# Kernel tuning notes

Measured on AMD Instinct MI355X. Metric: run time of the kernel, lower is better.

Reference implementation:

```python
import jax, jax.numpy as jnp
import numpy as np

N = 200000          # nodes
E = 800000          # edges (avg degree ~4, molecular graphs)
F_IN = 128          # dataset.num_node_features
HID = 32            # hidden_channels -> widths 32, 64, 128
N_TASKS = 128       # dataset.num_tasks
G = 8000            # number of graphs in the batch
EPS = 1e-5


def _glorot(key, shape):
    fan_in, fan_out = shape[0], shape[1]
    lim = np.sqrt(6.0 / (fan_in + fan_out)).astype(np.float32)
    return jax.random.uniform(key, shape, jnp.float32, -lim, lim)


def setup_inputs() -> dict:
    key = jax.random.key(0)
    ks = jax.random.split(key, 16)
    x = jax.random.normal(ks[0], (N, F_IN), jnp.float32)
    edge_index = jax.random.randint(ks[1], (2, E), 0, N, jnp.int64)
    batch = jnp.sort(jax.random.randint(ks[2], (N,), 0, G, jnp.int64))
    return {
        "x": x,
        "edge_index": edge_index,
        "batch": batch,
        "norm_w": jnp.ones((1,), jnp.float32),
        "norm_b": jnp.zeros((1,), jnp.float32),
        "W1": _glorot(ks[3], (F_IN, HID)),
        "b1": jnp.zeros((HID,), jnp.float32),
        "W2": _glorot(ks[4], (HID, 2 * HID)),
        "b2": jnp.zeros((2 * HID,), jnp.float32),
        "W3": _glorot(ks[5], (2 * HID, 4 * HID)),
        "b3": jnp.zeros((4 * HID,), jnp.float32),
        "lin1_W": _glorot(ks[6], (4 * HID, 256)),
        "lin1_b": jnp.zeros((256,), jnp.float32),
        "lin2_W": _glorot(ks[7], (256, N_TASKS)),
        "lin2_b": jnp.zeros((N_TASKS,), jnp.float32),
    }


def _instance_norm(x, batch, w, b):
    # PyG InstanceNorm: per-graph, per-channel mean / biased var, scalar affine.
    ones = jnp.ones((x.shape[0], 1), x.dtype)
    cnt = jnp.maximum(jax.ops.segment_sum(ones, batch, num_segments=G), 1.0)  # [G,1]
    mean = jax.ops.segment_sum(x, batch, num_segments=G) / cnt               # [G,C]
    var = jax.ops.segment_sum(x * x, batch, num_segments=G) / cnt - mean * mean
    xn = (x - mean[batch]) * jax.lax.rsqrt(var[batch] + EPS)
    return xn * w + b


def _gcn_conv(x, src, dst, dis, W, b):
    # GCNConv: h = xW; out_i = sum_j (d_i d_j)^{-1/2} h_j over A+I edges; + bias.
    h = x @ W
    msg = h[src] * (dis[src] * dis[dst])[:, None]          # [E, C] gather
    agg = jax.ops.segment_sum(msg, dst, num_segments=x.shape[0])
    agg = agg + h * (dis * dis)[:, None]                   # self-loop term
    return agg + b


def reference(x, edge_index, batch, norm_w, norm_b, W1, b1, W2, b2, W3, b3,
              lin1_W, lin1_b, lin2_W, lin2_b):
    src, dst = edge_index[0], edge_index[1]
    # degrees on A + I (all edge weights 1)
    deg = 1.0 + jax.ops.segment_sum(jnp.ones((E,), x.dtype), dst, num_segments=N)
    dis = jax.lax.rsqrt(deg)                                # deg >= 1, safe

    h = _instance_norm(x, batch, norm_w, norm_b)
    h = jax.nn.relu(_gcn_conv(h, src, dst, dis, W1, b1))
    h = jax.nn.relu(_gcn_conv(h, src, dst, dis, W2, b2))
    h = jax.nn.relu(_gcn_conv(h, src, dst, dis, W3, b3))

    # global_max_pool; empty graphs -> 0 (values are >=0 post-relu)
    pooled = jnp.maximum(jax.ops.segment_max(h, batch, num_segments=G), 0.0)

    out = jax.nn.relu(pooled @ lin1_W + lin1_b)
    return out @ lin2_W + lin2_b
```

## Files before the change

### kernel.cpp

```cpp
#include <hip/hip_runtime.h>
#include <hip/hip_bf16.h>
#include <stdint.h>

#define NN 200000
#define NE 800000
#define FIN 128
#define NG 8000
#define EPSV 1e-5f
#define NBS ((NN + 255) / 256)

typedef __attribute__((ext_vector_type(8))) short bf16x8;
typedef __attribute__((ext_vector_type(4))) float f32x4;

static __device__ __forceinline__ bf16x8 as_bf16x8(uint4 u) {
    union { uint4 u; bf16x8 v; } c; c.u = u; return c.v;
}

static __device__ __forceinline__ void u2f(uint4 v, float4& lo, float4& hi) {
    lo.x = __uint_as_float(v.x << 16); lo.y = __uint_as_float(v.x & 0xffff0000u);
    lo.z = __uint_as_float(v.y << 16); lo.w = __uint_as_float(v.y & 0xffff0000u);
    hi.x = __uint_as_float(v.z << 16); hi.y = __uint_as_float(v.z & 0xffff0000u);
    hi.z = __uint_as_float(v.w << 16); hi.w = __uint_as_float(v.w & 0xffff0000u);
}
static __device__ __forceinline__ unsigned int pk(float a, float b) {
    __hip_bfloat16 x = __float2bfloat16(a), y = __float2bfloat16(b);
    return (unsigned int)(*(unsigned short*)&x) | ((unsigned int)(*(unsigned short*)&y) << 16);
}

__global__ void k_cnt(const int* __restrict__ dst, int* __restrict__ cnt) {
    int e = blockIdx.x * 256 + threadIdx.x;
    if (e < NE) atomicAdd(&cnt[dst[e]], 1);
}

__global__ void k_blocksum(const int* __restrict__ cnt, int* __restrict__ bsum) {
    __shared__ int sh[256];
    int b = blockIdx.x, t = threadIdx.x;
    int idx = b * 256 + t;
    sh[t] = (idx < NN) ? cnt[idx] : 0;
    __syncthreads();
    for (int o = 128; o > 0; o >>= 1) {
        if (t < o) sh[t] += sh[t + o];
        __syncthreads();
    }
    if (t == 0) bsum[b] = sh[0];
}

__global__ __launch_bounds__(1024) void k_scanb(const int* __restrict__ bsum, int* __restrict__ bpre) {
    __shared__ int sh[1024];
    int t = threadIdx.x;
    int v = (t < NBS) ? bsum[t] : 0;
    sh[t] = v;
    __syncthreads();
    for (int o = 1; o < 1024; o <<= 1) {
        int add = (t >= o) ? sh[t - o] : 0;
        __syncthreads();
        sh[t] += add;
        __syncthreads();
    }
    if (t < NBS) bpre[t] = sh[t] - v;
}

__global__ void k_scanchunk(const int* __restrict__ cnt, const int* __restrict__ bpre,
                            int* __restrict__ rowstart) {
    __shared__ int sh[256];
    int b = blockIdx.x, t = threadIdx.x;
    int idx = b * 256 + t;
    int v = (idx < NN) ? cnt[idx] : 0;
    sh[t] = v;
    __syncthreads();
    for (int o = 1; o < 256; o <<= 1) {
        int add = (t >= o) ? sh[t - o] : 0;
        __syncthreads();
        sh[t] += add;
        __syncthreads();
    }
    if (idx < NN) rowstart[idx] = bpre[b] + sh[t] - v;
    if (idx == 0) rowstart[NN] = NE;
}

__global__ void k_dis(int* __restrict__ cnt) {
    int n = blockIdx.x * 256 + threadIdx.x;
    if (n < NN) {
        float d = rsqrtf(1.0f + (float)cnt[n]);
        ((float*)cnt)[n] = d;
    }
}

__global__ void k_fill(const int* __restrict__ src, const int* __restrict__ dst,
                       int* __restrict__ cursor, int* __restrict__ csr) {
    int e = blockIdx.x * 256 + threadIdx.x;
    if (e < NE) {
        int pos = atomicAdd(&cursor[dst[e]], 1);
        csr[pos] = src[e];
    }
}

__global__ void k_starts(const int* __restrict__ batch, int* __restrict__ startg) {
    int n = blockIdx.x * 256 + threadIdx.x;
    if (n >= NN) return;
    int b = batch[n];
    int prev = (n == 0) ? -1 : batch[n - 1];
    for (int g = prev + 1; g <= b; ++g) startg[g] = n;
    if (n == NN - 1) {
        for (int g = b + 1; g <= NG; ++g) startg[g] = NN;
    }
}

__global__ __launch_bounds__(256) void k_w3split(const float* __restrict__ W3,
                                                 unsigned short* __restrict__ whi,
                                                 unsigned short* __restrict__ wlo) {
    int i = blockIdx.x * 256 + threadIdx.x;
    if (i >= 64 * 128) return;
    int n = i >> 6, k = i & 63;
    float w = W3[k * 128 + n];
    __hip_bfloat16 h = __float2bfloat16(w);
    float hf = __bfloat162float(h);
    __hip_bfloat16 l = __float2bfloat16(w - hf);
    whi[n * 64 + k] = *(unsigned short*)&h;
    wlo[n * 64 + k] = *(unsigned short*)&l;
}

__global__ __launch_bounds__(256) void k_stats2(const float* __restrict__ x,
                                                const int* __restrict__ startg,
                                                const float* __restrict__ nw,
                                                const float* __restrict__ nb,
                                                float* __restrict__ scale,
                                                float* __restrict__ shift) {
    __shared__ float4 rsum[256], rsq[256];
    int g = blockIdx.x;
    int s = startg[g], e = startg[g + 1];
    if (s == e) return;
    int t = threadIdx.x;
    int slot = t >> 5, c4 = t & 31;
    const float4* x4 = (const float4*)x;
    float4 sum = {0.f, 0.f, 0.f, 0.f}, sq = {0.f, 0.f, 0.f, 0.f};
    for (int n = s + slot; n < e; n += 8) {
        float4 v = x4[n * 32 + c4];
        sum.x += v.x; sum.y += v.y; sum.z += v.z; sum.w += v.w;
        sq.x += v.x * v.x; sq.y += v.y * v.y; sq.z += v.z * v.z; sq.w += v.w * v.w;
    }
    rsum[slot * 32 + c4] = sum;
    rsq[slot * 32 + c4] = sq;
    __syncthreads();
    if (t < 32) {
        float4 S = rsum[t], Q = rsq[t];
#pragma unroll
        for (int sl = 1; sl < 8; ++sl) {
            float4 a = rsum[sl * 32 + t], b = rsq[sl * 32 + t];
            S.x += a.x; S.y += a.y; S.z += a.z; S.w += a.w;
            Q.x += b.x; Q.y += b.y; Q.z += b.z; Q.w += b.w;
        }
        float inv = 1.0f / (float)(e - s);
        float w = nw[0], b = nb[0];
        float4 sc, sh;
        {
            float m = S.x * inv, v = fmaxf(Q.x * inv - m * m, 0.f);
            float is = rsqrtf(v + EPSV); sc.x = is * w; sh.x = b - m * is * w;
        }
        {
            float m = S.y * inv, v = fmaxf(Q.y * inv - m * m, 0.f);
            float is = rsqrtf(v + EPSV); sc.y = is * w; sh.y = b - m * is * w;
        }
        {
            float m = S.z * inv, v = fmaxf(Q.z * inv - m * m, 0.f);
            float is = rsqrtf(v + EPSV); sc.z = is * w; sh.z = b - m * is * w;
        }
        {
            float m = S.w * inv, v = fmaxf(Q.w * inv - m * m, 0.f);
            float is = rsqrtf(v + EPSV); sc.w = is * w; sh.w = b - m * is * w;
        }
        ((float4*)scale)[g * 32 + t] = sc;
        ((float4*)shift)[g * 32 + t] = sh;
    }
}

__global__ __launch_bounds__(256) void k_conv1s(const float* __restrict__ x,
                                                const int* __restrict__ batch,
                                                const float* __restrict__ scale,
                                                const float* __restrict__ shift,
                                                const float* __restrict__ W1,
                                                const float* __restrict__ dis,
                                                float* __restrict__ p1) {
    __shared__ float4 sx4[64 * 33];
    int t = threadIdx.x;
    int base = blockIdx.x * 64;
    const float4* x4 = (const float4*)x;
    const float4* sc4 = (const float4*)scale;
    const float4* sh4 = (const float4*)shift;
    for (int i = t; i < 64 * 32; i += 256) {
        int nl = i >> 5, c4 = i & 31;
        int n = base + nl;
        int g = batch[n];
        float4 xv = x4[n * 32 + c4];
        float4 sc = sc4[g * 32 + c4];
        float4 sh = sh4[g * 32 + c4];
        float4 r;
        r.x = fmaf(xv.x, sc.x, sh.x);
        r.y = fmaf(xv.y, sc.y, sh.y);
        r.z = fmaf(xv.z, sc.z, sh.z);
        r.w = fmaf(xv.w, sc.w, sh.w);
        sx4[nl * 33 + c4] = r;
    }
    __syncthreads();
    int lane = t & 63;
    int kq = __builtin_amdgcn_readfirstlane(t >> 6) * 2;
    const float4* W4 = (const float4*)W1;
    const float4* arow = &sx4[lane * 33];
    float4 acc0 = {0.f, 0.f, 0.f, 0.f}, acc1 = {0.f, 0.f, 0.f, 0.f};
#pragma unroll 4
    for (int c4 = 0; c4 < 32; ++c4) {
        float4 a = arow[c4];
        int rb = c4 * 32 + kq;
        float4 wA0 = W4[rb +  0], wA1 = W4[rb +  1];
        float4 wB0 = W4[rb +  8], wB1 = W4[rb +  9];
        float4 wC0 = W4[rb + 16], wC1 = W4[rb + 17];
        float4 wD0 = W4[rb + 24], wD1 = W4[rb + 25];
        acc0.x += a.x * wA0.x + a.y * wB0.x + a.z * wC0.x + a.w * wD0.x;
        acc0.y += a.x * wA0.y + a.y * wB0.y + a.z * wC0.y + a.w * wD0.y;
        acc0.z += a.x * wA0.z + a.y * wB0.z + a.z * wC0.z + a.w * wD0.z;
        acc0.w += a.x * wA0.w + a.y * wB0.w + a.z * wC0.w + a.w * wD0.w;
        acc1.x += a.x * wA1.x + a.y * wB1.x + a.z * wC1.x + a.w * wD1.x;
        acc1.y += a.x * wA1.y + a.y * wB1.y + a.z * wC1.y + a.w * wD1.y;
        acc1.z += a.x * wA1.z + a.y * wB1.z + a.z * wC1.z + a.w * wD1.z;
        acc1.w += a.x * wA1.w + a.y * wB1.w + a.z * wC1.w + a.w * wD1.w;
    }
    int n = base + lane;
    float d = dis[n];
    float4 r0, r1;
    r0.x = acc0.x * d; r0.y = acc0.y * d; r0.z = acc0.z * d; r0.w = acc0.w * d;
    r1.x = acc1.x * d; r1.y = acc1.y * d; r1.z = acc1.z * d; r1.w = acc1.w * d;
    ((float4*)p1)[n * 8 + kq] = r0;
    ((float4*)p1)[n * 8 + kq + 1] = r1;
}

__global__ __launch_bounds__(256) void k_gather1(const float* __restrict__ p1,
                                                 const int* __restrict__ rowstart,
                                                 const int* __restrict__ csr,
                                                 const float* __restrict__ dis,
                                                 const float* __restrict__ b1,
                                                 float* __restrict__ p2) {
    int tid = blockIdx.x * 256 + threadIdx.x;
    int n = tid >> 3, c4 = tid & 7;
    const float4* p1_4 = (const float4*)p1;
    int s = rowstart[n], e = rowstart[n + 1];
    float4 agg = p1_4[n * 8 + c4];
    int j = s;
    for (; j + 1 < e; j += 2) {
        float4 v0 = p1_4[csr[j] * 8 + c4];
        float4 v1 = p1_4[csr[j + 1] * 8 + c4];
        agg.x += v0.x + v1.x; agg.y += v0.y + v1.y;
        agg.z += v0.z + v1.z; agg.w += v0.w + v1.w;
    }
    if (j < e) {
        float4 v = p1_4[csr[j] * 8 + c4];
        agg.x += v.x; agg.y += v.y; agg.z += v.z; agg.w += v.w;
    }
    float d = dis[n];
    float4 bb = ((const float4*)b1)[c4];
    float4 r;
    r.x = fmaxf(d * agg.x + bb.x, 0.f) * d;
    r.y = fmaxf(d * agg.y + bb.y, 0.f) * d;
    r.z = fmaxf(d * agg.z + bb.z, 0.f) * d;
    r.w = fmaxf(d * agg.w + bb.w, 0.f) * d;
    ((float4*)p2)[n * 8 + c4] = r;
}

__global__ __launch_bounds__(256) void k_conv2g(const float* __restrict__ p2,
                                                const int* __restrict__ rowstart,
                                                const int* __restrict__ csr,
                                                const float* __restrict__ dis,
                                                const float* __restrict__ W2,
                                                const float* __restrict__ b2v,
                                                __hip_bfloat16* __restrict__ p3h) {
    __shared__ float sW[32 * 64];
    __shared__ float4 spart[16 * 16];
    __shared__ float sa[16 * 32];
    int t = threadIdx.x;
    const float4* W4 = (const float4*)W2;
    for (int i = t; i < 32 * 64 / 4; i += 256) ((float4*)sW)[i] = W4[i];
    int base = blockIdx.x * 16;
    const float4* p2_4 = (const float4*)p2;
    {
        int node = t >> 4, c4 = t & 7, half = (t >> 3) & 1;
        int n = base + node;
        int s = rowstart[n], e = rowstart[n + 1];
        float4 agg = {0.f, 0.f, 0.f, 0.f};
        if (half == 0) {
            agg = p2_4[n * 8 + c4];
            for (int j = s; j < e; j += 2) {
                float4 v = p2_4[csr[j] * 8 + c4];
                agg.x += v.x; agg.y += v.y; agg.z += v.z; agg.w += v.w;
            }
        } else {
            for (int j = s + 1; j < e; j += 2) {
                float4 v = p2_4[csr[j] * 8 + c4];
                agg.x += v.x; agg.y += v.y; agg.z += v.z; agg.w += v.w;
            }
        }
        spart[node * 16 + half * 8 + c4] = agg;
    }
    __syncthreads();
    if (t < 128) {
        int nd = t >> 3, cc = t & 7;
        float4 a = spart[nd * 16 + cc], b = spart[nd * 16 + 8 + cc];
        float d = dis[base + nd];
        float4 r;
        r.x = d * (a.x + b.x); r.y = d * (a.y + b.y);
        r.z = d * (a.z + b.z); r.w = d * (a.w + b.w);
        ((float4*)sa)[nd * 8 + cc] = r;
    }
    __syncthreads();
    int k = t & 63, grp = t >> 6;
    float acc[4] = {0.f, 0.f, 0.f, 0.f};
    for (int c = 0; c < 32; ++c) {
        float w = sW[c * 64 + k];
#pragma unroll
        for (int q = 0; q < 4; ++q) acc[q] += sa[(grp * 4 + q) * 32 + c] * w;
    }
    float bb = b2v[k];
#pragma unroll
    for (int q = 0; q < 4; ++q) {
        int n = base + grp * 4 + q;
        float h = fmaxf(acc[q] + bb, 0.f);
        p3h[n * 64 + k] = __float2bfloat16(h * dis[n]);
    }
}

__global__ __launch_bounds__(256) void k_gather3(const __hip_bfloat16* __restrict__ p3h,
                                                 const int* __restrict__ rowstart,
                                                 const int* __restrict__ csr,
                                                 const float* __restrict__ dis,
                                                 __hip_bfloat16* __restrict__ a3h) {
    int tid = blockIdx.x * 256 + threadIdx.x;
    int n = tid >> 3, c8 = tid & 7;
    const uint4* p3q = (const uint4*)p3h;
    int s = rowstart[n], e = rowstart[n + 1];
    float4 alo, ahi;
    u2f(p3q[n * 8 + c8], alo, ahi);
    int j = s;
    for (; j + 1 < e; j += 2) {
        float4 l0, h0, l1, h1;
        u2f(p3q[csr[j] * 8 + c8], l0, h0);
        u2f(p3q[csr[j + 1] * 8 + c8], l1, h1);
        alo.x += l0.x + l1.x; alo.y += l0.y + l1.y;
        alo.z += l0.z + l1.z; alo.w += l0.w + l1.w;
        ahi.x += h0.x + h1.x; ahi.y += h0.y + h1.y;
        ahi.z += h0.z + h1.z; ahi.w += h0.w + h1.w;
    }
    if (j < e) {
        float4 l0, h0;
        u2f(p3q[csr[j] * 8 + c8], l0, h0);
        alo.x += l0.x; alo.y += l0.y; alo.z += l0.z; alo.w += l0.w;
        ahi.x += h0.x; ahi.y += h0.y; ahi.z += h0.z; ahi.w += h0.w;
    }
    float d = dis[n];
    uint4 o;
    o.x = pk(d * alo.x, d * alo.y);
    o.y = pk(d * alo.z, d * alo.w);
    o.z = pk(d * ahi.x, d * ahi.y);
    o.w = pk(d * ahi.z, d * ahi.w);
    ((uint4*)a3h)[n * 8 + c8] = o;
}

__global__ __launch_bounds__(256) void k_conv3m(const __hip_bfloat16* __restrict__ a3h,
                                                const unsigned short* __restrict__ w3hi,
                                                const unsigned short* __restrict__ w3lo,
                                                const float* __restrict__ b3v,
                                                const int* __restrict__ batch,
                                                unsigned int* __restrict__ pooled) {
    __shared__ uint4 sa[64 * 9];
    __shared__ float sp[64 * 132];
    __shared__ int sbatch[64];
    int t = threadIdx.x;
    int base = blockIdx.x * 64;
    if (t < 64) sbatch[t] = batch[base + t];
    const uint4* a3q = (const uint4*)a3h;
    for (int i = t; i < 64 * 8; i += 256) {
        sa[(i >> 3) * 9 + (i & 7)] = a3q[(size_t)base * 8 + i];
    }
    __syncthreads();
    int lane = t & 63, w = t >> 6;
    int h = lane >> 4;
    int cid = lane & 15;
    const uint4* WHq = (const uint4*)w3hi;
    const uint4* WLq = (const uint4*)w3lo;
    uint4 bh[2][2], bl[2][2];
#pragma unroll
    for (int nl = 0; nl < 2; ++nl) {
        int n = (w * 2 + nl) * 16 + cid;
#pragma unroll
        for (int kt = 0; kt < 2; ++kt) {
            bh[nl][kt] = WHq[n * 8 + kt * 4 + h];
            bl[nl][kt] = WLq[n * 8 + kt * 4 + h];
        }
    }
    f32x4 acc[2][4];
#pragma unroll
    for (int nl = 0; nl < 2; ++nl)
#pragma unroll
        for (int mi = 0; mi < 4; ++mi) acc[nl][mi] = {0.f, 0.f, 0.f, 0.f};
#pragma unroll
    for (int mi = 0; mi < 4; ++mi) {
        int arow = (mi * 16 + cid) * 9;
        bf16x8 a0 = as_bf16x8(sa[arow + h]);
        bf16x8 a1 = as_bf16x8(sa[arow + 4 + h]);
#pragma unroll
        for (int nl = 0; nl < 2; ++nl) {
            acc[nl][mi] = __builtin_amdgcn_mfma_f32_16x16x32_bf16(a0, as_bf16x8(bh[nl][0]), acc[nl][mi], 0, 0, 0);
            acc[nl][mi] = __builtin_amdgcn_mfma_f32_16x16x32_bf16(a1, as_bf16x8(bh[nl][1]), acc[nl][mi], 0, 0, 0);
            acc[nl][mi] = __builtin_amdgcn_mfma_f32_16x16x32_bf16(a0, as_bf16x8(bl[nl][0]), acc[nl][mi], 0, 0, 0);
            acc[nl][mi] = __builtin_amdgcn_mfma_f32_16x16x32_bf16(a1, as_bf16x8(bl[nl][1]), acc[nl][mi], 0, 0, 0);
        }
    }
#pragma unroll
    for (int nl = 0; nl < 2; ++nl) {
        int ch = (w * 2 + nl) * 16 + cid;
        float bb = b3v[ch];
#pragma unroll
        for (int mi = 0; mi < 4; ++mi) {
#pragma unroll
            for (int r = 0; r < 4; ++r) {
                int node_l = mi * 16 + h * 4 + r;
                sp[node_l * 132 + ch] = fmaxf(acc[nl][mi][r] + bb, 0.f);
            }
        }
    }
    __syncthreads();
    int k4 = t & 31, n0 = (t >> 5) * 8;
    int curg = sbatch[n0];
    float4 cm = {0.f, 0.f, 0.f, 0.f};
#pragma unroll
    for (int ii = 0; ii < 8; ++ii) {
        int g = sbatch[n0 + ii];
        float4 hv = *(const float4*)&sp[(n0 + ii) * 132 + k4 * 4];
        if (g != curg) {
            atomicMax(&pooled[curg * 128 + k4 * 4 + 0], __float_as_uint(cm.x));
            atomicMax(&pooled[curg * 128 + k4 * 4 + 1], __float_as_uint(cm.y));
            atomicMax(&pooled[curg * 128 + k4 * 4 + 2], __float_as_uint(cm.z));
            atomicMax(&pooled[curg * 128 + k4 * 4 + 3], __float_as_uint(cm.w));
            cm = {0.f, 0.f, 0.f, 0.f};
            curg = g;
        }
        cm.x = fmaxf(cm.x, hv.x);
        cm.y = fmaxf(cm.y, hv.y);
        cm.z = fmaxf(cm.z, hv.z);
        cm.w = fmaxf(cm.w, hv.w);
    }
    atomicMax(&pooled[curg * 128 + k4 * 4 + 0], __float_as_uint(cm.x));
    atomicMax(&pooled[curg * 128 + k4 * 4 + 1], __float_as_uint(cm.y));
    atomicMax(&pooled[curg * 128 + k4 * 4 + 2], __float_as_uint(cm.z));
    atomicMax(&pooled[curg * 128 + k4 * 4 + 3], __float_as_uint(cm.w));
}

__global__ __launch_bounds__(256) void k_lin1(const float* __restrict__ pooled,
                                              const float* __restrict__ W,
                                              const float* __restrict__ bias,
                                              float* __restrict__ mid) {
    __shared__ float sp[8 * 128];
    int t = threadIdx.x;
    int base = blockIdx.x * 8;
    for (int i = t; i < 8 * 128; i += 256) sp[i] = pooled[base * 128 + i];
    __syncthreads();
    float acc[8] = {0.f, 0.f, 0.f, 0.f, 0.f, 0.f, 0.f, 0.f};
    for (int c = 0; c < 128; ++c) {
        float w = W[c * 256 + t];
#pragma unroll
        for (int gl = 0; gl < 8; ++gl) acc[gl] += sp[gl * 128 + c] * w;
    }
    float bb = bias[t];
#pragma unroll
    for (int gl = 0; gl < 8; ++gl) mid[(base + gl) * 256 + t] = fmaxf(acc[gl] + bb, 0.f);
}

__global__ __launch_bounds__(128) void k_lin2(const float* __restrict__ mid,
                                              const float* __restrict__ W,
                                              const float* __restrict__ bias,
                                              float* __restrict__ out) {
    __shared__ float sm[16 * 256];
    int t = threadIdx.x;
    int base = blockIdx.x * 16;
    for (int i = t; i < 16 * 256; i += 128) sm[i] = mid[base * 256 + i];
    __syncthreads();
    float acc[16];
#pragma unroll
    for (int i = 0; i < 16; ++i) acc[i] = 0.f;
    for (int c = 0; c < 256; ++c) {
        float w = W[c * 128 + t];
#pragma unroll
        for (int gl = 0; gl < 16; ++gl) acc[gl] += sm[gl * 256 + c] * w;
    }
    float bb = bias[t];
#pragma unroll
    for (int gl = 0; gl < 16; ++gl)
        out[(base + gl) * 128 + t] = acc[gl] + bb;
}

extern "C" void kernel_launch(void* const* d_in, const int* in_sizes, int n_in,
                              void* d_out, int out_size, void* d_ws, size_t ws_size,
                              hipStream_t stream) {
    (void)in_sizes; (void)n_in; (void)out_size; (void)ws_size;
    const float* x   = (const float*)d_in[0];
    const int* ei    = (const int*)d_in[1];
    const int* src = ei;
    const int* dst = ei + NE;
    const int* batch = (const int*)d_in[2];
    const float* nw  = (const float*)d_in[3];
    const float* nb  = (const float*)d_in[4];
    const float* W1  = (const float*)d_in[5];
    const float* b1  = (const float*)d_in[6];
    const float* W2  = (const float*)d_in[7];
    const float* b2  = (const float*)d_in[8];
    const float* W3  = (const float*)d_in[9];
    const float* b3  = (const float*)d_in[10];
    const float* l1W = (const float*)d_in[11];
    const float* l1b = (const float*)d_in[12];
    const float* l2W = (const float*)d_in[13];
    const float* l2b = (const float*)d_in[14];
    float* out = (float*)d_out;

    char* wsp = (char*)d_ws;
    int*   cnt      = (int*)wsp;   wsp += (size_t)NN * 4;
    int*   rowstart = (int*)wsp;   wsp += (size_t)(NN + 1) * 4;
    int*   cursor   = (int*)wsp;   wsp += (size_t)NN * 4;
    int*   bsum     = (int*)wsp;   wsp += (size_t)NBS * 4;
    int*   bpre     = (int*)wsp;   wsp += (size_t)NBS * 4;
    int*   startg   = (int*)wsp;   wsp += (size_t)(NG + 1) * 4;
    int*   csr      = (int*)wsp;   wsp += (size_t)NE * 4;
    wsp += ((256 - ((uintptr_t)wsp & 255)) & 255);
    unsigned short* w3hi = (unsigned short*)wsp; wsp += (size_t)128 * 64 * 2;
    unsigned short* w3lo = (unsigned short*)wsp; wsp += (size_t)128 * 64 * 2;
    float* scale   = (float*)wsp; wsp += (size_t)NG * 128 * 4;
    float* shift   = (float*)wsp; wsp += (size_t)NG * 128 * 4;
    float* pooled  = (float*)wsp; wsp += (size_t)NG * 128 * 4;
    float* regionA = (float*)wsp; wsp += (size_t)NN * 64 * 4;
    float* regionB = (float*)wsp; wsp += (size_t)NN * 64 * 4;

    float* dis  = (float*)cnt;
    float* p1   = regionA;
    float* p2   = regionA + (size_t)NN * 32;
    __hip_bfloat16* p3h = (__hip_bfloat16*)regionB;
    __hip_bfloat16* a3h = (__hip_bfloat16*)regionA;
    float* mid  = regionB;

    hipMemsetAsync(cnt, 0, (size_t)NN * 4, stream);
    k_cnt<<<(NE + 255) / 256, 256, 0, stream>>>(dst, cnt);
    k_blocksum<<<NBS, 256, 0, stream>>>(cnt, bsum);
    k_scanb<<<1, 1024, 0, stream>>>(bsum, bpre);
    k_scanchunk<<<NBS, 256, 0, stream>>>(cnt, bpre, rowstart);
    k_dis<<<(NN + 255) / 256, 256, 0, stream>>>(cnt);
    hipMemcpyAsync(cursor, rowstart, (size_t)NN * 4, hipMemcpyDeviceToDevice, stream);
    k_fill<<<(NE + 255) / 256, 256, 0, stream>>>(src, dst, cursor, csr);
    k_w3split<<<32, 256, 0, stream>>>(W3, w3hi, w3lo);

    k_starts<<<(NN + 255) / 256, 256, 0, stream>>>(batch, startg);
    k_stats2<<<NG, 256, 0, stream>>>(x, startg, nw, nb, scale, shift);
    k_conv1s<<<NN / 64, 256, 0, stream>>>(x, batch, scale, shift, W1, dis, p1);
    k_gather1<<<NN * 8 / 256, 256, 0, stream>>>(p1, rowstart, csr, dis, b1, p2);
    k_conv2g<<<NN / 16, 256, 0, stream>>>(p2, rowstart, csr, dis, W2, b2, p3h);
    k_gather3<<<NN * 8 / 256, 256, 0, stream>>>(p3h, rowstart, csr, dis, a3h);
    hipMemsetAsync(pooled, 0, (size_t)NG * 128 * 4, stream);
    k_conv3m<<<NN / 64, 256, 0, stream>>>(a3h, w3hi, w3lo, b3, batch, (unsigned int*)pooled);

    k_lin1<<<NG / 8, 256, 0, stream>>>(pooled, l1W, l1b, mid);
    k_lin2<<<NG / 16, 128, 0, stream>>>(mid, l2W, l2b, out);
}
```

Baseline: 532.0 us.

## Fuse dis and cursor init into scan, pool interior graphs in LDS, retile MLP

Folds the degree-rsqrt kernel and the cursor memcpy into the chunk-scan kernel, removing one launch and one device copy. In the conv3 max-pool epilogue, graphs fully contained within a 64-node tile are reduced with LDS atomics and written directly, and only boundary graphs use global atomicMax. The lin1 and lin2 kernels process twice as many graphs per block to reuse weight loads, at the cost of more registers. The LDS pool buffer reuses the sa shared array and assumes at most 16 interior graphs per tile.

```diff
diff --git a/kernel.cpp b/kernel.cpp
--- a/kernel.cpp
+++ b/kernel.cpp
@@ -60,8 +60,8 @@
     if (t < NBS) bpre[t] = sh[t] - v;
 }
 
-__global__ void k_scanchunk(const int* __restrict__ cnt, const int* __restrict__ bpre,
-                            int* __restrict__ rowstart) {
+__global__ void k_scanchunk(int* __restrict__ cnt, const int* __restrict__ bpre,
+                            int* __restrict__ rowstart, int* __restrict__ cursor) {
     __shared__ int sh[256];
     int b = blockIdx.x, t = threadIdx.x;
     int idx = b * 256 + t;
@@ -74,16 +74,13 @@
         sh[t] += add;
         __syncthreads();
     }
-    if (idx < NN) rowstart[idx] = bpre[b] + sh[t] - v;
+    if (idx < NN) {
+        int rs = bpre[b] + sh[t] - v;
+        rowstart[idx] = rs;
+        cursor[idx] = rs;
+        ((float*)cnt)[idx] = rsqrtf(1.0f + (float)v);
+    }
     if (idx == 0) rowstart[NN] = NE;
-}
-
-__global__ void k_dis(int* __restrict__ cnt) {
-    int n = blockIdx.x * 256 + threadIdx.x;
-    if (n < NN) {
-        float d = rsqrtf(1.0f + (float)cnt[n]);
-        ((float*)cnt)[n] = d;
-    }
 }
 
 __global__ void k_fill(const int* __restrict__ src, const int* __restrict__ dst,
@@ -426,6 +423,10 @@
         }
     }
     __syncthreads();
+    unsigned int* spool = (unsigned int*)sa;
+    for (int i = t; i < 16 * 128; i += 256) spool[i] = 0u;
+    __syncthreads();
+    int g0 = sbatch[0], g63 = sbatch[63];
     int k4 = t & 31, n0 = (t >> 5) * 8;
     int curg = sbatch[n0];
     float4 cm = {0.f, 0.f, 0.f, 0.f};
@@ -434,10 +435,20 @@
         int g = sbatch[n0 + ii];
         float4 hv = *(const float4*)&sp[(n0 + ii) * 132 + k4 * 4];
         if (g != curg) {
-            atomicMax(&pooled[curg * 128 + k4 * 4 + 0], __float_as_uint(cm.x));
-            atomicMax(&pooled[curg * 128 + k4 * 4 + 1], __float_as_uint(cm.y));
-            atomicMax(&pooled[curg * 128 + k4 * 4 + 2], __float_as_uint(cm.z));
-            atomicMax(&pooled[curg * 128 + k4 * 4 + 3], __float_as_uint(cm.w));
+            int s = curg - g0 - 1;
+            if (s >= 0 && curg < g63 && s < 16) {
+                unsigned int* d = spool + s * 128 + k4 * 4;
+                atomicMax(d + 0, __float_as_uint(cm.x));
+                atomicMax(d + 1, __float_as_uint(cm.y));
+                atomicMax(d + 2, __float_as_uint(cm.z));
+                atomicMax(d + 3, __float_as_uint(cm.w));
+            } else {
+                unsigned int* d = pooled + curg * 128 + k4 * 4;
+                atomicMax(d + 0, __float_as_uint(cm.x));
+                atomicMax(d + 1, __float_as_uint(cm.y));
+                atomicMax(d + 2, __float_as_uint(cm.z));
+                atomicMax(d + 3, __float_as_uint(cm.w));
+            }
             cm = {0.f, 0.f, 0.f, 0.f};
             curg = g;
         }
@@ -446,52 +457,80 @@
         cm.z = fmaxf(cm.z, hv.z);
         cm.w = fmaxf(cm.w, hv.w);
     }
-    atomicMax(&pooled[curg * 128 + k4 * 4 + 0], __float_as_uint(cm.x));
-    atomicMax(&pooled[curg * 128 + k4 * 4 + 1], __float_as_uint(cm.y));
-    atomicMax(&pooled[curg * 128 + k4 * 4 + 2], __float_as_uint(cm.z));
-    atomicMax(&pooled[curg * 128 + k4 * 4 + 3], __float_as_uint(cm.w));
+    {
+        int s = curg - g0 - 1;
+        if (s >= 0 && curg < g63 && s < 16) {
+            unsigned int* d = spool + s * 128 + k4 * 4;
+            atomicMax(d + 0, __float_as_uint(cm.x));
+            atomicMax(d + 1, __float_as_uint(cm.y));
+            atomicMax(d + 2, __float_as_uint(cm.z));
+            atomicMax(d + 3, __float_as_uint(cm.w));
+        } else {
+            unsigned int* d = pooled + curg * 128 + k4 * 4;
+            atomicMax(d + 0, __float_as_uint(cm.x));
+            atomicMax(d + 1, __float_as_uint(cm.y));
+            atomicMax(d + 2, __float_as_uint(cm.z));
+            atomicMax(d + 3, __float_as_uint(cm.w));
+        }
+    }
+    __syncthreads();
+    {
+        int s = t >> 4;
+        int g = g0 + 1 + s;
+        if (g < g63) {
+            int ch = (t & 15) * 8;
+            const float* spf = (const float*)spool;
+            float4 v0 = *(const float4*)&spf[s * 128 + ch];
+            float4 v1 = *(const float4*)&spf[s * 128 + ch + 4];
+            float4* pf = (float4*)pooled;
+            pf[g * 32 + (ch >> 2)] = v0;
+            pf[g * 32 + (ch >> 2) + 1] = v1;
+        }
+    }
 }
 
 __global__ __launch_bounds__(256) void k_lin1(const float* __restrict__ pooled,
                                               const float* __restrict__ W,
                                               const float* __restrict__ bias,
                                               float* __restrict__ mid) {
-    __shared__ float sp[8 * 128];
+    __shared__ float sp[16 * 128];
     int t = threadIdx.x;
-    int base = blockIdx.x * 8;
-    for (int i = t; i < 8 * 128; i += 256) sp[i] = pooled[base * 128 + i];
-    __syncthreads();
-    float acc[8] = {0.f, 0.f, 0.f, 0.f, 0.f, 0.f, 0.f, 0.f};
+    int base = blockIdx.x * 16;
+    for (int i = t; i < 16 * 128; i += 256) sp[i] = pooled[base * 128 + i];
+    __syncthreads();
+    float acc[16];
+#pragma unroll
+    for (int i = 0; i < 16; ++i) acc[i] = 0.f;
     for (int c = 0; c < 128; ++c) {
         float w = W[c * 256 + t];
 #pragma unroll
-        for (int gl = 0; gl < 8; ++gl) acc[gl] += sp[gl * 128 + c] * w;
+        for (int gl = 0; gl < 16; ++gl) acc[gl] += sp[gl * 128 + c] * w;
     }
     float bb = bias[t];
 #pragma unroll
-    for (int gl = 0; gl < 8; ++gl) mid[(base + gl) * 256 + t] = fmaxf(acc[gl] + bb, 0.f);
+    for (int gl = 0; gl < 16; ++gl) mid[(base + gl) * 256 + t] = fmaxf(acc[gl] + bb, 0.f);
 }
 
 __global__ __launch_bounds__(128) void k_lin2(const float* __restrict__ mid,
                                               const float* __restrict__ W,
                                               const float* __restrict__ bias,
                                               float* __restrict__ out) {
-    __shared__ float sm[16 * 256];
+    __shared__ float sm[32 * 256];
     int t = threadIdx.x;
-    int base = blockIdx.x * 16;
-    for (int i = t; i < 16 * 256; i += 128) sm[i] = mid[base * 256 + i];
-    __syncthreads();
-    float acc[16];
-#pragma unroll
-    for (int i = 0; i < 16; ++i) acc[i] = 0.f;
+    int base = blockIdx.x * 32;
+    for (int i = t; i < 32 * 256; i += 128) sm[i] = mid[base * 256 + i];
+    __syncthreads();
+    float acc[32];
+#pragma unroll
+    for (int i = 0; i < 32; ++i) acc[i] = 0.f;
     for (int c = 0; c < 256; ++c) {
         float w = W[c * 128 + t];
 #pragma unroll
-        for (int gl = 0; gl < 16; ++gl) acc[gl] += sm[gl * 256 + c] * w;
+        for (int gl = 0; gl < 32; ++gl) acc[gl] += sm[gl * 256 + c] * w;
     }
     float bb = bias[t];
 #pragma unroll
-    for (int gl = 0; gl < 16; ++gl)
+    for (int gl = 0; gl < 32; ++gl)
         out[(base + gl) * 128 + t] = acc[gl] + bb;
 }
 
@@ -546,9 +585,7 @@
     k_cnt<<<(NE + 255) / 256, 256, 0, stream>>>(dst, cnt);
     k_blocksum<<<NBS, 256, 0, stream>>>(cnt, bsum);
     k_scanb<<<1, 1024, 0, stream>>>(bsum, bpre);
-    k_scanchunk<<<NBS, 256, 0, stream>>>(cnt, bpre, rowstart);
-    k_dis<<<(NN + 255) / 256, 256, 0, stream>>>(cnt);
-    hipMemcpyAsync(cursor, rowstart, (size_t)NN * 4, hipMemcpyDeviceToDevice, stream);
+    k_scanchunk<<<NBS, 256, 0, stream>>>(cnt, bpre, rowstart, cursor);
     k_fill<<<(NE + 255) / 256, 256, 0, stream>>>(src, dst, cursor, csr);
     k_w3split<<<32, 256, 0, stream>>>(W3, w3hi, w3lo);
 
@@ -561,6 +598,6 @@
     hipMemsetAsync(pooled, 0, (size_t)NG * 128 * 4, stream);
     k_conv3m<<<NN / 64, 256, 0, stream>>>(a3h, w3hi, w3lo, b3, batch, (unsigned int*)pooled);
 
-    k_lin1<<<NG / 8, 256, 0, stream>>>(pooled, l1W, l1b, mid);
-    k_lin2<<<NG / 16, 128, 0, stream>>>(mid, l2W, l2b, out);
-}
+    k_lin1<<<NG / 16, 256, 0, stream>>>(pooled, l1W, l1b, mid);
+    k_lin2<<<NG / 32, 128, 0, stream>>>(mid, l2W, l2b, out);
+}
```

After: 540.3 us. No clear change (+1.6%).
